# Performance work log

Measured on AMD Instinct MI355X. Metric: run time of the kernel, lower is better.

Reference implementation:

```python
import jax, jax.numpy as jnp
import numpy as np

B, T, F, H, E = 256, 512, 32, 512, 32
NUM_TICKERS, PREDICT_DAYS = 5000, 30


def setup_inputs() -> dict:
    key = jax.random.key(0)
    ks = jax.random.split(key, 16)
    s = 0.05  # small init scale for stability
    return {
        "ticker_id": jax.random.randint(ks[0], (B,), 0, NUM_TICKERS),
        "sequence": jax.random.normal(ks[1], (B, T, F), jnp.float32),
        "embed_table": jax.random.normal(ks[2], (NUM_TICKERS, E), jnp.float32) * s,
        "Wih0": jax.random.normal(ks[3], (3 * H, F), jnp.float32) * s,
        "Whh0": jax.random.normal(ks[4], (3 * H, H), jnp.float32) * s,
        "bih0": jax.random.normal(ks[5], (3 * H,), jnp.float32) * s,
        "bhh0": jax.random.normal(ks[6], (3 * H,), jnp.float32) * s,
        "Wih1": jax.random.normal(ks[7], (3 * H, H), jnp.float32) * s,
        "Whh1": jax.random.normal(ks[8], (3 * H, H), jnp.float32) * s,
        "bih1": jax.random.normal(ks[9], (3 * H,), jnp.float32) * s,
        "bhh1": jax.random.normal(ks[10], (3 * H,), jnp.float32) * s,
        "fc1_w": jax.random.normal(ks[11], (H, H + E), jnp.float32) * s,
        "fc1_b": jax.random.normal(ks[12], (H,), jnp.float32) * s,
        "fc2_w": jax.random.normal(ks[13], (PREDICT_DAYS, H), jnp.float32) * s,
        "fc2_b": jax.random.normal(ks[14], (PREDICT_DAYS,), jnp.float32) * s,
    }


def _gru_layer(x, Wih, Whh, bih, bhh):
    """Standard torch-convention GRU layer. x: (B,T,in) -> (B,T,H), h_last (B,H).
    Gate packing along 3H axis: [r, z, n]."""
    Hs = Whh.shape[1]
    # precompute input projections for all timesteps in one GEMM
    gx = jnp.einsum('btf,gf->tbg', x, Wih) + bih  # (T,B,3H)

    def step(h, gxt):
        gh = h @ Whh.T + bhh                         # (B,3H)
        r = jax.nn.sigmoid(gxt[:, :Hs] + gh[:, :Hs])
        z = jax.nn.sigmoid(gxt[:, Hs:2 * Hs] + gh[:, Hs:2 * Hs])
        n = jnp.tanh(gxt[:, 2 * Hs:] + r * gh[:, 2 * Hs:])
        h_new = (1.0 - z) * n + z * h
        return h_new, h_new

    h0 = jnp.zeros((x.shape[0], Hs), x.dtype)
    h_last, ys = jax.lax.scan(step, h0, gx)          # ys: (T,B,H)
    return jnp.moveaxis(ys, 0, 1), h_last


def reference(ticker_id, sequence, embed_table, Wih0, Whh0, bih0, bhh0,
              Wih1, Whh1, bih1, bhh1, fc1_w, fc1_b, fc2_w, fc2_b):
    out0, _ = _gru_layer(sequence, Wih0, Whh0, bih0, bhh0)
    _, h_last = _gru_layer(out0, Wih1, Whh1, bih1, bhh1)   # top-layer final hidden (B,H)
    embed = embed_table[ticker_id]                          # (B,E)
    h = jnp.concatenate([h_last, embed], axis=1)            # (B,H+E)
    h = jax.nn.relu(h @ fc1_w.T + fc1_b)                    # dropout is eval no-op
    return h @ fc2_w.T + fc2_b                              # (B, predict_days)
```

## Files before the change

### kernel.cpp

```cpp
#include <hip/hip_runtime.h>
#include <hip/hip_bf16.h>


namespace {
constexpr int kB  = 256;
constexpr int kT  = 512;
constexpr int kF  = 32;
constexpr int kH  = 512;
constexpr int kE  = 32;
constexpr int kPD = 30;

constexpr int GBLK = 256;
constexpr int NTHR = 256;
constexpr int RG   = 32;
constexpr int HB   = 16;

constexpr int IMG  = kB * kH * 2;
constexpr int RING = 8;

constexpr int PART_OFF = 0;
constexpr int PARTN    = 1536;
constexpr int LDSB     = 98304;
static_assert(LDSB <= 160 * 1024, "LDS overflow");

constexpr size_t WS_CNT   = 0;
constexpr size_t WS_TOTAL = 1024;
constexpr size_t WS_FB    = 1152;
constexpr size_t WS_FLG1  = 2048;
constexpr size_t WS_FLG0  = 4096;
constexpr size_t WS_H0B   = 65536;
constexpr size_t WS_H1B   = WS_H0B + (size_t)RING * IMG;
constexpr size_t WS_H1F   = WS_H1B + (size_t)RING * IMG;
constexpr size_t WS_INIT  = WS_H1F;

typedef __bf16 bf16_t;
typedef __bf16 bf16x8 __attribute__((ext_vector_type(8)));
typedef float  f32x4  __attribute__((ext_vector_type(4)));

#define MFMA __builtin_amdgcn_mfma_f32_16x16x32_bf16
#define LDSF4(p) (*(__attribute__((address_space(3))) f32x4*)(p))

#define WAITVM(N)                                              \
  do {                                                         \
    asm volatile("s_waitcnt vmcnt(" #N ")" ::: "memory");      \
    __builtin_amdgcn_sched_barrier(0);                         \
  } while (0)

__device__ __forceinline__ float sigmoid_f(float x) {
  return 1.f / (1.f + __expf(-x));
}
__device__ __forceinline__ float tanh_f(float x) {
  float a = fabsf(x);
  float e = __expf(-2.f * a);
  float t = (1.f - e) / (1.f + e);
  return copysignf(t, x);
}

__device__ __forceinline__ bf16x8 ld16a(const char* p) {
  bf16x8 v;
  asm volatile("global_load_dwordx4 %0, %1, off"
               : "=v"(v) : "v"(p) : "memory");
  return v;
}

__device__ __forceinline__ bf16x8 fragf(const float* p) {
  bf16x8 t;
#pragma unroll
  for (int j = 0; j < 8; ++j) t[j] = (bf16_t)p[j];
  return t;
}

__device__ __forceinline__ bf16x8 ld16_mall(const bf16_t* p) {
  const unsigned long long* q = (const unsigned long long*)p;
  unsigned long long lo =
      __hip_atomic_load(q, __ATOMIC_RELAXED, __HIP_MEMORY_SCOPE_AGENT);
  unsigned long long hi =
      __hip_atomic_load(q + 1, __ATOMIC_RELAXED, __HIP_MEMORY_SCOPE_AGENT);
  union { unsigned long long u[2]; bf16x8 v; } x;
  x.u[0] = lo; x.u[1] = hi;
  return x.v;
}

__device__ __forceinline__ void st2_mall(bf16_t* p, float v) {
  bf16_t b = (bf16_t)v;
  unsigned short bits = __builtin_bit_cast(unsigned short, b);
  __hip_atomic_store((unsigned short*)p, bits, __ATOMIC_RELAXED,
                     __HIP_MEMORY_SCOPE_AGENT);
}
template <bool XL>
__device__ __forceinline__ void st2x(bf16_t* p, float v) {
  if constexpr (XL) *p = (bf16_t)v;
  else st2_mall(p, v);
}

__device__ __forceinline__ void drain_stores() {
  asm volatile("s_waitcnt vmcnt(0)" ::: "memory");
}

__device__ __forceinline__ unsigned ld_flag_sc1(const unsigned* p) {
  unsigned v;
  asm volatile("global_load_dword %0, %1, off sc1\n\ts_waitcnt vmcnt(0)"
               : "=v"(v) : "v"(p) : "memory");
  return v;
}

template <bool XL>
__device__ __forceinline__ void poll_flags(const unsigned* base, int idx,
                                           unsigned tgt) {
  const unsigned* fp = base + idx;
  long guard = 0;
  if constexpr (XL) {
    for (;;) {
      unsigned v = ld_flag_sc1(fp);
      if (__all((int)(v >= tgt))) break;
      if (++guard > (1L << 22)) break;
    }
  } else {
    for (;;) {
      unsigned v = __hip_atomic_load(fp, __ATOMIC_RELAXED,
                                     __HIP_MEMORY_SCOPE_AGENT);
      if (__all((int)(v >= tgt))) break;
      __builtin_amdgcn_s_sleep(1);
      if (++guard > (1L << 20)) break;
    }
  }
}

template <bool XL>
__device__ __forceinline__ void flag_post(unsigned* p, unsigned tgt) {
  if constexpr (XL) {
    *(volatile unsigned*)p = tgt;
  } else {
    __hip_atomic_store(p, tgt, __ATOMIC_RELAXED, __HIP_MEMORY_SCOPE_AGENT);
  }
}
}


#define L0_ISSUE(buf, base)                                         \
  _Pragma("unroll") for (int j = 0; j < 4; ++j)                     \
      buf[j] = ld16a(hsrc + (base + j) * 1024)
#define L0_MFMA(buf, base)                                          \
  _Pragma("unroll") for (int j = 0; j < 4; ++j) {                   \
    aR  = MFMA(buf[j], f0[0][base + j], aR, 0, 0, 0);               \
    aZ  = MFMA(buf[j], f0[1][base + j], aZ, 0, 0, 0);               \
    aNH = MFMA(buf[j], f0[2][base + j], aNH, 0, 0, 0);              \
  }
#define L1_ISSUE(b0, b1, base)                                      \
  _Pragma("unroll") for (int j = 0; j < 4; ++j) {                   \
    b0[j] = ld16a(hsrc + (base + j) * 1024);                        \
    b1[j] = ld16a(hsrc + 16384 + (base + j) * 1024);                \
  }
#define L1_MFMA(acc0, acc1, acc2, w, b0, b1, base)                  \
  _Pragma("unroll") for (int j = 0; j < 4; ++j) {                   \
    acc0[0] = MFMA(b0[j], w[0][base + j], acc0[0], 0, 0, 0);        \
    acc0[1] = MFMA(b1[j], w[0][base + j], acc0[1], 0, 0, 0);        \
    acc1[0] = MFMA(b0[j], w[1][base + j], acc1[0], 0, 0, 0);        \
    acc1[1] = MFMA(b1[j], w[1][base + j], acc1[1], 0, 0, 0);        \
    acc2[0] = MFMA(b0[j], w[2][base + j], acc2[0], 0, 0, 0);        \
    acc2[1] = MFMA(b1[j], w[2][base + j], acc2[1], 0, 0, 0);        \
  }

template <bool XL>
__device__ __attribute__((noinline)) void role_l0(
    const float* __restrict__ seq, const float* __restrict__ Whh0,
    const float* __restrict__ Wih0, bf16_t* __restrict__ h0b,
    unsigned* __restrict__ flg0p, int g, int slot, int lane, int rbase,
    int rt, int c, float b0r, float b0z, float b0nx, float b0nh) {
  const int lm = lane & 15, lq = lane >> 4, koff = lq * 8;
  const int arow = rbase + rt * 16 + lm;

  bf16x8 f0[3][17];
#pragma unroll
  for (int gg = 0; gg < 3; ++gg) {
    const float* wh = Whh0 + (size_t)(gg * kH + c) * kH + koff;
#pragma unroll
    for (int kc = 0; kc < 16; ++kc) f0[gg][kc] = fragf(wh + kc * 32);
    f0[gg][16] = fragf(Wih0 + (size_t)(gg * kH + c) * kF + koff);
  }
  float h0m[4] = {0.f, 0.f, 0.f, 0.f};

  const int kcb = slot >> 1;
  const int lq2 = ((slot & 1) << 1) | (lm >> 3);
  const int stoff = ((g * 2 + rt) * 16 + kcb) * 1024 +
                    ((lq2 << 4) + lq * 4) * 16 + (lm & 7) * 2;
  const int tbase = (g * 2 + rt) * 16 * 1024;

  for (int s = 0; s <= kT; ++s) {
    const int pr = (s + RING - 1) & (RING - 1), pw = s & (RING - 1);
    if (s < kT) {
      const float* xp = seq + ((size_t)arow * kT + s) * kF + koff;
      float xs[8];
#pragma unroll
      for (int j = 0; j < 8; ++j) xs[j] = xp[j];
      if (s > 0) poll_flags<XL>(flg0p, lane, (unsigned)s);
      if constexpr (XL) {
        if ((s & (RING - 1)) == 0) asm volatile("buffer_inv" ::: "memory");
      }
      f32x4 aR{0,0,0,0}, aZ{0,0,0,0}, aNH{0,0,0,0}, aNX{0,0,0,0};
      const char* hsrc = (const char*)h0b + pr * IMG + tbase + lane * 16;
      if constexpr (XL) {
        bf16x8 cA[4], cB[4];
        L0_ISSUE(cA, 0);
        L0_ISSUE(cB, 4);
        WAITVM(4);
        L0_MFMA(cA, 0);
        L0_ISSUE(cA, 8);
        WAITVM(4);
        L0_MFMA(cB, 4);
        L0_ISSUE(cB, 12);
        WAITVM(4);
        L0_MFMA(cA, 8);
        WAITVM(0);
        L0_MFMA(cB, 12);
      } else {
#pragma unroll
        for (int kc = 0; kc < 16; ++kc) {
          bf16x8 a = ld16_mall((const bf16_t*)(hsrc + kc * 1024));
          aR  = MFMA(a, f0[0][kc], aR, 0, 0, 0);
          aZ  = MFMA(a, f0[1][kc], aZ, 0, 0, 0);
          aNH = MFMA(a, f0[2][kc], aNH, 0, 0, 0);
        }
      }
      {
        bf16x8 ax;
#pragma unroll
        for (int j = 0; j < 8; ++j) ax[j] = (bf16_t)xs[j];
        aR  = MFMA(ax, f0[0][16], aR, 0, 0, 0);
        aZ  = MFMA(ax, f0[1][16], aZ, 0, 0, 0);
        aNX = MFMA(ax, f0[2][16], aNX, 0, 0, 0);
      }
      char* hnb = (char*)h0b + pw * IMG;
#pragma unroll
      for (int i = 0; i < 4; ++i) {
        float r = sigmoid_f(aR[i] + b0r);
        float z = sigmoid_f(aZ[i] + b0z);
        float n = tanh_f((aNX[i] + b0nx) + r * (aNH[i] + b0nh));
        float hn = (1.f - z) * n + z * h0m[i];
        h0m[i] = hn;
        st2x<XL>((bf16_t*)(hnb + stoff + i * 16), hn);
      }
      drain_stores();
      if (lane == 0) flag_post<XL>(flg0p + rt * 32 + slot, (unsigned)(s + 1));
    }
    __syncthreads();
    if constexpr (!XL) __syncthreads();
  }
}

template <bool XL>
__device__ __attribute__((noinline)) void role_l1h(
    const float* __restrict__ Whh1, bf16_t* __restrict__ h1b,
    float* __restrict__ h1f, unsigned* __restrict__ flg1p, int slot,
    float* part, int g, int lane, int rbase, int c,
    float b1r, float b1z, float b1nx, float b1nh) {
  const int lm = lane & 15, lq = lane >> 4, koff = lq * 8;
  bf16x8 fh[3][16];
#pragma unroll
  for (int gg = 0; gg < 3; ++gg) {
    const float* wh = Whh1 + (size_t)(gg * kH + c) * kH + koff;
#pragma unroll
    for (int kc = 0; kc < 16; ++kc) fh[gg][kc] = fragf(wh + kc * 32);
  }
  float h1m[2][4] = {{0,0,0,0},{0,0,0,0}};

  const int kcb = slot >> 1;
  const int lq2 = ((slot & 1) << 1) | (lm >> 3);
  const int st0 = (g * 2 * 16 + kcb) * 1024 +
                  ((lq2 << 4) + lq * 4) * 16 + (lm & 7) * 2;
  const int tbase = g * 2 * 16 * 1024;

  for (int s = 0; s <= kT; ++s) {
    const int pr = (s + RING - 1) & (RING - 1), pw = s & (RING - 1);
    f32x4 cR[2], cZ[2], cNH[2];
#pragma unroll
    for (int rt = 0; rt < 2; ++rt) {
      cR[rt] = f32x4{0,0,0,0}; cZ[rt] = f32x4{0,0,0,0}; cNH[rt] = f32x4{0,0,0,0};
    }
    if (s >= 1) {
      poll_flags<XL>(flg1p, lane & 31, (unsigned)s);
      if constexpr (XL) {
        if ((s & (RING - 1)) == 0) asm volatile("buffer_inv" ::: "memory");
      }
      const char* hsrc = (const char*)h1b + pr * IMG + tbase + lane * 16;
      if constexpr (XL) {
        bf16x8 a0A[4], a1A[4], a0B[4], a1B[4];
        L1_ISSUE(a0A, a1A, 0);
        L1_ISSUE(a0B, a1B, 4);
        WAITVM(8);
        L1_MFMA(cR, cZ, cNH, fh, a0A, a1A, 0);
        L1_ISSUE(a0A, a1A, 8);
        WAITVM(8);
        L1_MFMA(cR, cZ, cNH, fh, a0B, a1B, 4);
        L1_ISSUE(a0B, a1B, 12);
        WAITVM(8);
        L1_MFMA(cR, cZ, cNH, fh, a0A, a1A, 8);
        WAITVM(0);
        L1_MFMA(cR, cZ, cNH, fh, a0B, a1B, 12);
      } else {
#pragma unroll
        for (int kc = 0; kc < 16; ++kc) {
          bf16x8 a0 = ld16_mall((const bf16_t*)(hsrc + kc * 1024));
          bf16x8 a1 = ld16_mall((const bf16_t*)(hsrc + 16384 + kc * 1024));
          cR[0]  = MFMA(a0, fh[0][kc], cR[0], 0,0,0);
          cR[1]  = MFMA(a1, fh[0][kc], cR[1], 0,0,0);
          cZ[0]  = MFMA(a0, fh[1][kc], cZ[0], 0,0,0);
          cZ[1]  = MFMA(a1, fh[1][kc], cZ[1], 0,0,0);
          cNH[0] = MFMA(a0, fh[2][kc], cNH[0],0,0,0);
          cNH[1] = MFMA(a1, fh[2][kc], cNH[1],0,0,0);
        }
      }
    }
    __syncthreads();
    if (s >= 1) {
      float* pb = part + (s & 1) * PARTN;
      char* hnb = (char*)h1b + pw * IMG;
#pragma unroll
      for (int rt = 0; rt < 2; ++rt) {
        f32x4 pR  = LDSF4(pb + ((rt * 3 + 0) * 64 + lane) * 4);
        f32x4 pZ  = LDSF4(pb + ((rt * 3 + 1) * 64 + lane) * 4);
        f32x4 pNX = LDSF4(pb + ((rt * 3 + 2) * 64 + lane) * 4);
#pragma unroll
        for (int i = 0; i < 4; ++i) {
          float r = sigmoid_f(cR[rt][i] + pR[i] + b1r);
          float z = sigmoid_f(cZ[rt][i] + pZ[i] + b1z);
          float n = tanh_f((pNX[i] + b1nx) + r * (cNH[rt][i] + b1nh));
          float hn = (1.f - z) * n + z * h1m[rt][i];
          h1m[rt][i] = hn;
          if (s < kT) st2x<XL>((bf16_t*)(hnb + st0 + rt * 16384 + i * 16), hn);
          else        h1f[(rbase + rt * 16 + lq * 4 + i) * kH + c] = hn;
        }
      }
    }
    if (s < kT) {
      drain_stores();
      if (lane == 0) flag_post<XL>(flg1p + slot, (unsigned)(s + 1));
    }
    if constexpr (!XL) {
      if (s < kT) poll_flags<XL>(flg1p, lane & 31, (unsigned)(s + 1));
      __syncthreads();
    }
  }
}

template <bool XL>
__device__ __attribute__((noinline)) void role_l1x(
    const float* __restrict__ Wih1, bf16_t* __restrict__ h0b,
    float* part, unsigned* __restrict__ flg0p, int g, int lane, int c) {
  const int lq = lane >> 4, koff = lq * 8;
  bf16x8 fx[3][16];
#pragma unroll
  for (int gg = 0; gg < 3; ++gg) {
    const float* wi = Wih1 + (size_t)(gg * kH + c) * kH + koff;
#pragma unroll
    for (int kc = 0; kc < 16; ++kc) fx[gg][kc] = fragf(wi + kc * 32);
  }
  const int tbase = g * 2 * 16 * 1024;

  for (int s = 0; s <= kT; ++s) {
    const int pr = (s + RING - 1) & (RING - 1);
    if (s >= 1) {
      poll_flags<XL>(flg0p, lane, (unsigned)s);
      if constexpr (XL) {
        if ((s & (RING - 1)) == 0) asm volatile("buffer_inv" ::: "memory");
      }
      f32x4 xR[2], xZ[2], xNX[2];
#pragma unroll
      for (int rt = 0; rt < 2; ++rt) {
        xR[rt] = f32x4{0,0,0,0}; xZ[rt] = f32x4{0,0,0,0}; xNX[rt] = f32x4{0,0,0,0};
      }
      const char* hsrc = (const char*)h0b + pr * IMG + tbase + lane * 16;
      if constexpr (XL) {
        bf16x8 a0A[4], a1A[4], a0B[4], a1B[4];
        L1_ISSUE(a0A, a1A, 0);
        L1_ISSUE(a0B, a1B, 4);
        WAITVM(8);
        L1_MFMA(xR, xZ, xNX, fx, a0A, a1A, 0);
        L1_ISSUE(a0A, a1A, 8);
        WAITVM(8);
        L1_MFMA(xR, xZ, xNX, fx, a0B, a1B, 4);
        L1_ISSUE(a0B, a1B, 12);
        WAITVM(8);
        L1_MFMA(xR, xZ, xNX, fx, a0A, a1A, 8);
        WAITVM(0);
        L1_MFMA(xR, xZ, xNX, fx, a0B, a1B, 12);
      } else {
#pragma unroll
        for (int kc = 0; kc < 16; ++kc) {
          bf16x8 a0 = ld16_mall((const bf16_t*)(hsrc + kc * 1024));
          bf16x8 a1 = ld16_mall((const bf16_t*)(hsrc + 16384 + kc * 1024));
          xR[0]  = MFMA(a0, fx[0][kc], xR[0], 0,0,0);
          xR[1]  = MFMA(a1, fx[0][kc], xR[1], 0,0,0);
          xZ[0]  = MFMA(a0, fx[1][kc], xZ[0], 0,0,0);
          xZ[1]  = MFMA(a1, fx[1][kc], xZ[1], 0,0,0);
          xNX[0] = MFMA(a0, fx[2][kc], xNX[0],0,0,0);
          xNX[1] = MFMA(a1, fx[2][kc], xNX[1],0,0,0);
        }
      }
      float* pb = part + (s & 1) * PARTN;
#pragma unroll
      for (int rt = 0; rt < 2; ++rt) {
        LDSF4(pb + ((rt * 3 + 0) * 64 + lane) * 4) = xR[rt];
        LDSF4(pb + ((rt * 3 + 1) * 64 + lane) * 4) = xZ[rt];
        LDSF4(pb + ((rt * 3 + 2) * 64 + lane) * 4) = xNX[rt];
      }
    }
    __syncthreads();
    if constexpr (!XL) __syncthreads();
  }
}

__launch_bounds__(NTHR, 1)
__global__ void gru_persistent(
    const float* __restrict__ seq,
    const float* __restrict__ Wih0, const float* __restrict__ Whh0,
    const float* __restrict__ bih0, const float* __restrict__ bhh0,
    const float* __restrict__ Wih1, const float* __restrict__ Whh1,
    const float* __restrict__ bih1, const float* __restrict__ bhh1,
    char* __restrict__ ws) {
  extern __shared__ char smem[];
  float* part = (float*)(smem + PART_OFF);
  __shared__ unsigned sh_enc;

  const int tid = threadIdx.x;

  if (tid == 0) {
    unsigned xcd;
    asm("s_getreg_b32 %0, hwreg(HW_REG_XCC_ID)" : "=s"(xcd));
    xcd &= 7;
    unsigned* cnt   = (unsigned*)(ws + WS_CNT) + xcd * 32;
    unsigned* total = (unsigned*)(ws + WS_TOTAL);
    unsigned* fb    = (unsigned*)(ws + WS_FB);
    unsigned slot = __hip_atomic_fetch_add(cnt, 1u, __ATOMIC_RELAXED,
                                           __HIP_MEMORY_SCOPE_AGENT);
    if (slot >= 32)
      __hip_atomic_store(fb, 1u, __ATOMIC_RELAXED, __HIP_MEMORY_SCOPE_AGENT);
    __hip_atomic_fetch_add(total, 1u, __ATOMIC_RELAXED,
                           __HIP_MEMORY_SCOPE_AGENT);
    long guard = 0;
    while (__hip_atomic_load(total, __ATOMIC_RELAXED,
                             __HIP_MEMORY_SCOPE_AGENT) < (unsigned)GBLK) {
      __builtin_amdgcn_s_sleep(1);
      if (++guard > (1L << 24)) break;
    }
    unsigned f = __hip_atomic_load(fb, __ATOMIC_RELAXED,
                                   __HIP_MEMORY_SCOPE_AGENT);
    sh_enc = (f << 31) | (xcd << 8) | (slot & 255);
  }
  __syncthreads();
  const unsigned enc = sh_enc;
  const bool fallback = (enc >> 31) != 0;
  const int g    = fallback ? (blockIdx.x & 7)  : (int)((enc >> 8) & 7);
  const int slot = fallback ? (blockIdx.x >> 3) : (int)(enc & 255);
  const int hs   = slot * HB;

  const int lm = tid & 15;
  const int c = hs + lm;
  const float b0r  = bih0[c] + bhh0[c];
  const float b0z  = bih0[kH + c] + bhh0[kH + c];
  const float b0nx = bih0[2 * kH + c];
  const float b0nh = bhh0[2 * kH + c];
  const float b1r  = bih1[c] + bhh1[c];
  const float b1z  = bih1[kH + c] + bhh1[kH + c];
  const float b1nx = bih1[2 * kH + c];
  const float b1nh = bhh1[2 * kH + c];

  bf16_t* h0b = (bf16_t*)(ws + WS_H0B);
  bf16_t* h1b = (bf16_t*)(ws + WS_H1B);
  float*  h1f = (float*)(ws + WS_H1F);
  unsigned* flg1p = (unsigned*)(ws + WS_FLG1) + g * 32;
  unsigned* flg0p = (unsigned*)(ws + WS_FLG0) + g * 64;
  const int wv   = tid >> 6;
  const int lane = tid & 63;
  const int rbase = g * RG;

  if (!fallback) {
    if (wv == 0)
      role_l0<true>(seq, Whh0, Wih0, h0b, flg0p, g, slot, lane, rbase, 0, c,
                    b0r, b0z, b0nx, b0nh);
    else if (wv == 2)
      role_l0<true>(seq, Whh0, Wih0, h0b, flg0p, g, slot, lane, rbase, 1, c,
                    b0r, b0z, b0nx, b0nh);
    else if (wv == 1)
      role_l1h<true>(Whh1, h1b, h1f, flg1p, slot, part, g, lane, rbase, c,
                     b1r, b1z, b1nx, b1nh);
    else
      role_l1x<true>(Wih1, h0b, part, flg0p, g, lane, c);
  } else {
    if (wv == 0)
      role_l0<false>(seq, Whh0, Wih0, h0b, flg0p, g, slot, lane, rbase, 0, c,
                     b0r, b0z, b0nx, b0nh);
    else if (wv == 2)
      role_l0<false>(seq, Whh0, Wih0, h0b, flg0p, g, slot, lane, rbase, 1, c,
                     b0r, b0z, b0nx, b0nh);
    else if (wv == 1)
      role_l1h<false>(Whh1, h1b, h1f, flg1p, slot, part, g, lane, rbase, c,
                      b1r, b1z, b1nx, b1nh);
    else
      role_l1x<false>(Wih1, h0b, part, flg0p, g, lane, c);
  }
}

__global__ void head_kernel(const float* __restrict__ h1,
                            const int* __restrict__ ticker,
                            const float* __restrict__ etab,
                            const float* __restrict__ fc1w,
                            const float* __restrict__ fc1b,
                            const float* __restrict__ fc2w,
                            const float* __restrict__ fc2b,
                            float* __restrict__ out) {
  __shared__ float xin[4][kH + kE];
  __shared__ float y1[4][kH];
  const int tid = threadIdx.x;
  const int b0 = blockIdx.x * 4;

  for (int idx = tid; idx < 4 * (kH + kE); idx += 256) {
    const int r = idx / (kH + kE), k = idx % (kH + kE);
    const int b = b0 + r;
    xin[r][k] = (k < kH) ? h1[b * kH + k] : etab[ticker[b] * kE + (k - kH)];
  }
  __syncthreads();

#pragma unroll
  for (int jj = 0; jj < 2; ++jj) {
    const int j = tid + jj * 256;
    const float* wr = fc1w + j * (kH + kE);
    float a0 = 0.f, a1 = 0.f, a2 = 0.f, a3 = 0.f;
    for (int k = 0; k < kH + kE; ++k) {
      const float w = wr[k];
      a0 += w * xin[0][k];
      a1 += w * xin[1][k];
      a2 += w * xin[2][k];
      a3 += w * xin[3][k];
    }
    const float bb = fc1b[j];
    y1[0][j] = fmaxf(a0 + bb, 0.f);
    y1[1][j] = fmaxf(a1 + bb, 0.f);
    y1[2][j] = fmaxf(a2 + bb, 0.f);
    y1[3][j] = fmaxf(a3 + bb, 0.f);
  }
  __syncthreads();

  if (tid < 4 * kPD) {
    const int r = tid / kPD, j = tid % kPD;
    const float* wr = fc2w + j * kH;
    float acc = fc2b[j];
    for (int k = 0; k < kH; ++k) acc += wr[k] * y1[r][k];
    out[(b0 + r) * kPD + j] = acc;
  }
}

extern "C" void kernel_launch(void* const* d_in, const int* in_sizes, int n_in,
                              void* d_out, int out_size, void* d_ws,
                              size_t ws_size, hipStream_t stream) {
  (void)in_sizes; (void)n_in; (void)out_size; (void)ws_size;

  const int*   ticker = (const int*)d_in[0];
  const float* seq    = (const float*)d_in[1];
  const float* etab   = (const float*)d_in[2];
  const float* Wih0   = (const float*)d_in[3];
  const float* Whh0   = (const float*)d_in[4];
  const float* bih0   = (const float*)d_in[5];
  const float* bhh0   = (const float*)d_in[6];
  const float* Wih1   = (const float*)d_in[7];
  const float* Whh1   = (const float*)d_in[8];
  const float* bih1   = (const float*)d_in[9];
  const float* bhh1   = (const float*)d_in[10];
  const float* fc1w   = (const float*)d_in[11];
  const float* fc1b   = (const float*)d_in[12];
  const float* fc2w   = (const float*)d_in[13];
  const float* fc2b   = (const float*)d_in[14];

  char* ws = (char*)d_ws;
  (void)hipMemsetAsync(ws, 0, WS_INIT, stream);

  gru_persistent<<<GBLK, NTHR, LDSB, stream>>>(
      seq, Wih0, Whh0, bih0, bhh0, Wih1, Whh1, bih1, bhh1, ws);

  head_kernel<<<kB / 4, 256, 0, stream>>>((const float*)(ws + WS_H1F), ticker,
                                          etab, fc1w, fc1b, fc2w, fc2b,
                                          (float*)d_out);
}
```

Baseline: 2.178 ms.

## Split each recurrent role across two waves with LDS partial-sum handoff

Doubles the block to 512 threads and splits every role (layer-0 recurrence, layer-1 hidden and input projections) across a lead wave and a partner wave. Each wave handles half of the K dimension, and partner partial sums reach the lead through double-buffered LDS slots guarded by LDS mailbox counters. The aim is to halve the serial per-step MFMA and load chain on the latency-bound recurrence and to halve weight-fragment register pressure. The cost is extra LDS traffic and intra-block spin-wait handshakes on every timestep.

Measured after the change: 2.626 ms. 1.21x slower.

```diff
diff --git a/kernel.cpp b/kernel.cpp
--- a/kernel.cpp
+++ b/kernel.cpp
@@ -11,16 +11,19 @@
 constexpr int kPD = 30;
 
 constexpr int GBLK = 256;
-constexpr int NTHR = 256;
+constexpr int NTHR = 512;
 constexpr int RG   = 32;
 constexpr int HB   = 16;
 
 constexpr int IMG  = kB * kH * 2;
 constexpr int RING = 8;
 
-constexpr int PART_OFF = 0;
-constexpr int PARTN    = 1536;
-constexpr int LDSB     = 98304;
+constexpr int PB0_OFF = 0;
+constexpr int PB2_OFF = 8192;
+constexpr int PB1_OFF = 16384;
+constexpr int PB3_OFF = 32768;
+constexpr int HS_OFF  = 61440;
+constexpr int LDSB    = 98304;
 static_assert(LDSB <= 160 * 1024, "LDS overflow");
 
 constexpr size_t WS_CNT   = 0;
@@ -39,6 +42,7 @@
 
 #define MFMA __builtin_amdgcn_mfma_f32_16x16x32_bf16
 #define LDSF4(p) (*(__attribute__((address_space(3))) f32x4*)(p))
+#define LDSVU(p) (*(volatile __attribute__((address_space(3))) unsigned*)(p))
 
 #define WAITVM(N)                                              \
   do {                                                         \
@@ -134,24 +138,32 @@
     __hip_atomic_store(p, tgt, __ATOMIC_RELAXED, __HIP_MEMORY_SCOPE_AGENT);
   }
 }
-}
-
-
-#define L0_ISSUE(buf, base)                                         \
+
+__device__ __forceinline__ void lds_poll(unsigned* p, unsigned tgt) {
+  long guard = 0;
+  while (LDSVU(p) < tgt) {
+    if (++guard > (1L << 22)) break;
+  }
+  asm volatile("" ::: "memory");
+}
+}
+
+
+#define HL0_ISSUE(buf, base)                                        \
   _Pragma("unroll") for (int j = 0; j < 4; ++j)                     \
       buf[j] = ld16a(hsrc + (base + j) * 1024)
-#define L0_MFMA(buf, base)                                          \
+#define HL0_MFMA(w, buf, base)                                      \
   _Pragma("unroll") for (int j = 0; j < 4; ++j) {                   \
-    aR  = MFMA(buf[j], f0[0][base + j], aR, 0, 0, 0);               \
-    aZ  = MFMA(buf[j], f0[1][base + j], aZ, 0, 0, 0);               \
-    aNH = MFMA(buf[j], f0[2][base + j], aNH, 0, 0, 0);              \
-  }
-#define L1_ISSUE(b0, b1, base)                                      \
+    aR  = MFMA(buf[j], w[0][base + j], aR, 0, 0, 0);                \
+    aZ  = MFMA(buf[j], w[1][base + j], aZ, 0, 0, 0);                \
+    aNH = MFMA(buf[j], w[2][base + j], aNH, 0, 0, 0);               \
+  }
+#define HL1_ISSUE(b0, b1, base)                                     \
   _Pragma("unroll") for (int j = 0; j < 4; ++j) {                   \
     b0[j] = ld16a(hsrc + (base + j) * 1024);                        \
     b1[j] = ld16a(hsrc + 16384 + (base + j) * 1024);                \
   }
-#define L1_MFMA(acc0, acc1, acc2, w, b0, b1, base)                  \
+#define HL1_MFMA(acc0, acc1, acc2, w, b0, b1, base)                 \
   _Pragma("unroll") for (int j = 0; j < 4; ++j) {                   \
     acc0[0] = MFMA(b0[j], w[0][base + j], acc0[0], 0, 0, 0);        \
     acc0[1] = MFMA(b1[j], w[0][base + j], acc0[1], 0, 0, 0);        \
@@ -162,58 +174,97 @@
   }
 
 template <bool XL>
-__device__ __attribute__((noinline)) void role_l0(
+__device__ __attribute__((noinline)) void role_l0_lead(
     const float* __restrict__ seq, const float* __restrict__ Whh0,
     const float* __restrict__ Wih0, bf16_t* __restrict__ h0b,
-    unsigned* __restrict__ flg0p, int g, int slot, int lane, int rbase,
-    int rt, int c, float b0r, float b0z, float b0nx, float b0nh) {
+    unsigned* __restrict__ flg0p, unsigned* mb, unsigned* pd, float* pbuf,
+    int g, int slot, int lane, int rbase, int rt, int c,
+    float b0r, float b0z, float b0nx, float b0nh) {
   const int lm = lane & 15, lq = lane >> 4, koff = lq * 8;
   const int arow = rbase + rt * 16 + lm;
-
-  bf16x8 f0[3][17];
-#pragma unroll
-  for (int gg = 0; gg < 3; ++gg) {
-    const float* wh = Whh0 + (size_t)(gg * kH + c) * kH + koff;
-#pragma unroll
-    for (int kc = 0; kc < 16; ++kc) f0[gg][kc] = fragf(wh + kc * 32);
-    f0[gg][16] = fragf(Wih0 + (size_t)(gg * kH + c) * kF + koff);
-  }
-  float h0m[4] = {0.f, 0.f, 0.f, 0.f};
-
   const int kcb = slot >> 1;
   const int lq2 = ((slot & 1) << 1) | (lm >> 3);
   const int stoff = ((g * 2 + rt) * 16 + kcb) * 1024 +
                     ((lq2 << 4) + lq * 4) * 16 + (lm & 7) * 2;
   const int tbase = (g * 2 + rt) * 16 * 1024;
-
-  for (int s = 0; s <= kT; ++s) {
-    const int pr = (s + RING - 1) & (RING - 1), pw = s & (RING - 1);
-    if (s < kT) {
-      const float* xp = seq + ((size_t)arow * kT + s) * kF + koff;
-      float xs[8];
-#pragma unroll
-      for (int j = 0; j < 8; ++j) xs[j] = xp[j];
-      if (s > 0) poll_flags<XL>(flg0p, lane, (unsigned)s);
-      if constexpr (XL) {
+  float h0m[4] = {0.f, 0.f, 0.f, 0.f};
+
+  if constexpr (XL) {
+    bf16x8 f0[3][9];
+#pragma unroll
+    for (int gg = 0; gg < 3; ++gg) {
+      const float* wh = Whh0 + (size_t)(gg * kH + c) * kH + koff;
+#pragma unroll
+      for (int kc = 0; kc < 8; ++kc) f0[gg][kc] = fragf(wh + kc * 32);
+      f0[gg][8] = fragf(Wih0 + (size_t)(gg * kH + c) * kF + koff);
+    }
+    for (int s = 0; s <= kT; ++s) {
+      const int pr = (s + RING - 1) & (RING - 1), pw = s & (RING - 1);
+      if (s < kT) {
+        const float* xp = seq + ((size_t)arow * kT + s) * kF + koff;
+        float xs[8];
+#pragma unroll
+        for (int j = 0; j < 8; ++j) xs[j] = xp[j];
+        if (s > 0) poll_flags<XL>(flg0p, lane, (unsigned)s);
         if ((s & (RING - 1)) == 0) asm volatile("buffer_inv" ::: "memory");
-      }
-      f32x4 aR{0,0,0,0}, aZ{0,0,0,0}, aNH{0,0,0,0}, aNX{0,0,0,0};
-      const char* hsrc = (const char*)h0b + pr * IMG + tbase + lane * 16;
-      if constexpr (XL) {
+        if (lane == 0) LDSVU(mb) = (unsigned)(s + 1);
+        f32x4 aR{0,0,0,0}, aZ{0,0,0,0}, aNH{0,0,0,0}, aNX{0,0,0,0};
+        const char* hsrc = (const char*)h0b + pr * IMG + tbase + lane * 16;
         bf16x8 cA[4], cB[4];
-        L0_ISSUE(cA, 0);
-        L0_ISSUE(cB, 4);
+        HL0_ISSUE(cA, 0);
+        HL0_ISSUE(cB, 4);
         WAITVM(4);
-        L0_MFMA(cA, 0);
-        L0_ISSUE(cA, 8);
-        WAITVM(4);
-        L0_MFMA(cB, 4);
-        L0_ISSUE(cB, 12);
-        WAITVM(4);
-        L0_MFMA(cA, 8);
+        HL0_MFMA(f0, cA, 0);
         WAITVM(0);
-        L0_MFMA(cB, 12);
-      } else {
+        HL0_MFMA(f0, cB, 4);
+        {
+          bf16x8 ax;
+#pragma unroll
+          for (int j = 0; j < 8; ++j) ax[j] = (bf16_t)xs[j];
+          aR  = MFMA(ax, f0[0][8], aR, 0, 0, 0);
+          aZ  = MFMA(ax, f0[1][8], aZ, 0, 0, 0);
+          aNX = MFMA(ax, f0[2][8], aNX, 0, 0, 0);
+        }
+        lds_poll(pd, (unsigned)(s + 1));
+        float* pp = pbuf + (s & 1) * 768;
+        aR  += LDSF4(pp + (0 * 64 + lane) * 4);
+        aZ  += LDSF4(pp + (1 * 64 + lane) * 4);
+        aNH += LDSF4(pp + (2 * 64 + lane) * 4);
+        char* hnb = (char*)h0b + pw * IMG;
+#pragma unroll
+        for (int i = 0; i < 4; ++i) {
+          float r = sigmoid_f(aR[i] + b0r);
+          float z = sigmoid_f(aZ[i] + b0z);
+          float n = tanh_f((aNX[i] + b0nx) + r * (aNH[i] + b0nh));
+          float hn = (1.f - z) * n + z * h0m[i];
+          h0m[i] = hn;
+          st2x<XL>((bf16_t*)(hnb + stoff + i * 16), hn);
+        }
+        drain_stores();
+        if (lane == 0)
+          flag_post<XL>(flg0p + rt * 32 + slot, (unsigned)(s + 1));
+      }
+      __syncthreads();
+    }
+  } else {
+    bf16x8 f0[3][17];
+#pragma unroll
+    for (int gg = 0; gg < 3; ++gg) {
+      const float* wh = Whh0 + (size_t)(gg * kH + c) * kH + koff;
+#pragma unroll
+      for (int kc = 0; kc < 16; ++kc) f0[gg][kc] = fragf(wh + kc * 32);
+      f0[gg][16] = fragf(Wih0 + (size_t)(gg * kH + c) * kF + koff);
+    }
+    for (int s = 0; s <= kT; ++s) {
+      const int pr = (s + RING - 1) & (RING - 1), pw = s & (RING - 1);
+      if (s < kT) {
+        const float* xp = seq + ((size_t)arow * kT + s) * kF + koff;
+        float xs[8];
+#pragma unroll
+        for (int j = 0; j < 8; ++j) xs[j] = xp[j];
+        if (s > 0) poll_flags<XL>(flg0p, lane, (unsigned)s);
+        f32x4 aR{0,0,0,0}, aZ{0,0,0,0}, aNH{0,0,0,0}, aNX{0,0,0,0};
+        const char* hsrc = (const char*)h0b + pr * IMG + tbase + lane * 16;
 #pragma unroll
         for (int kc = 0; kc < 16; ++kc) {
           bf16x8 a = ld16_mall((const bf16_t*)(hsrc + kc * 1024));
@@ -221,83 +272,174 @@
           aZ  = MFMA(a, f0[1][kc], aZ, 0, 0, 0);
           aNH = MFMA(a, f0[2][kc], aNH, 0, 0, 0);
         }
-      }
-      {
         bf16x8 ax;
 #pragma unroll
         for (int j = 0; j < 8; ++j) ax[j] = (bf16_t)xs[j];
         aR  = MFMA(ax, f0[0][16], aR, 0, 0, 0);
         aZ  = MFMA(ax, f0[1][16], aZ, 0, 0, 0);
         aNX = MFMA(ax, f0[2][16], aNX, 0, 0, 0);
-      }
-      char* hnb = (char*)h0b + pw * IMG;
-#pragma unroll
-      for (int i = 0; i < 4; ++i) {
-        float r = sigmoid_f(aR[i] + b0r);
-        float z = sigmoid_f(aZ[i] + b0z);
-        float n = tanh_f((aNX[i] + b0nx) + r * (aNH[i] + b0nh));
-        float hn = (1.f - z) * n + z * h0m[i];
-        h0m[i] = hn;
-        st2x<XL>((bf16_t*)(hnb + stoff + i * 16), hn);
-      }
-      drain_stores();
-      if (lane == 0) flag_post<XL>(flg0p + rt * 32 + slot, (unsigned)(s + 1));
-    }
-    __syncthreads();
-    if constexpr (!XL) __syncthreads();
+        char* hnb = (char*)h0b + pw * IMG;
+#pragma unroll
+        for (int i = 0; i < 4; ++i) {
+          float r = sigmoid_f(aR[i] + b0r);
+          float z = sigmoid_f(aZ[i] + b0z);
+          float n = tanh_f((aNX[i] + b0nx) + r * (aNH[i] + b0nh));
+          float hn = (1.f - z) * n + z * h0m[i];
+          h0m[i] = hn;
+          st2x<XL>((bf16_t*)(hnb + stoff + i * 16), hn);
+        }
+        drain_stores();
+        if (lane == 0)
+          flag_post<XL>(flg0p + rt * 32 + slot, (unsigned)(s + 1));
+      }
+      __syncthreads();
+      __syncthreads();
+    }
   }
 }
 
 template <bool XL>
-__device__ __attribute__((noinline)) void role_l1h(
+__device__ __attribute__((noinline)) void role_l0_part(
+    const float* __restrict__ Whh0, bf16_t* __restrict__ h0b,
+    unsigned* mb, unsigned* pd, float* pbuf,
+    int g, int lane, int rt, int c) {
+  if constexpr (XL) {
+    const int lq = lane >> 4, koff = lq * 8;
+    bf16x8 f4[3][8];
+#pragma unroll
+    for (int gg = 0; gg < 3; ++gg) {
+      const float* wh = Whh0 + (size_t)(gg * kH + c) * kH + koff;
+#pragma unroll
+      for (int kc = 0; kc < 8; ++kc) f4[gg][kc] = fragf(wh + (8 + kc) * 32);
+    }
+    const int tbase = (g * 2 + rt) * 16 * 1024;
+    for (int s = 0; s <= kT; ++s) {
+      const int pr = (s + RING - 1) & (RING - 1);
+      if (s < kT) {
+        lds_poll(mb, (unsigned)(s + 1));
+        if ((s & (RING - 1)) == 0) asm volatile("buffer_inv" ::: "memory");
+        f32x4 aR{0,0,0,0}, aZ{0,0,0,0}, aNH{0,0,0,0};
+        const char* hsrc =
+            (const char*)h0b + pr * IMG + tbase + 8192 + lane * 16;
+        bf16x8 cA[4], cB[4];
+        HL0_ISSUE(cA, 0);
+        HL0_ISSUE(cB, 4);
+        WAITVM(4);
+        HL0_MFMA(f4, cA, 0);
+        WAITVM(0);
+        HL0_MFMA(f4, cB, 4);
+        float* pp = pbuf + (s & 1) * 768;
+        LDSF4(pp + (0 * 64 + lane) * 4) = aR;
+        LDSF4(pp + (1 * 64 + lane) * 4) = aZ;
+        LDSF4(pp + (2 * 64 + lane) * 4) = aNH;
+        asm volatile("s_waitcnt lgkmcnt(0)" ::: "memory");
+        if (lane == 0) LDSVU(pd) = (unsigned)(s + 1);
+      }
+      __syncthreads();
+    }
+  } else {
+    for (int s = 0; s <= kT; ++s) { __syncthreads(); __syncthreads(); }
+  }
+}
+
+template <bool XL>
+__device__ __attribute__((noinline)) void role_l1h_lead(
     const float* __restrict__ Whh1, bf16_t* __restrict__ h1b,
     float* __restrict__ h1f, unsigned* __restrict__ flg1p, int slot,
-    float* part, int g, int lane, int rbase, int c,
+    float* p1b, float* p3b, unsigned* mb, int g, int lane, int rbase, int c,
     float b1r, float b1z, float b1nx, float b1nh) {
   const int lm = lane & 15, lq = lane >> 4, koff = lq * 8;
-  bf16x8 fh[3][16];
-#pragma unroll
-  for (int gg = 0; gg < 3; ++gg) {
-    const float* wh = Whh1 + (size_t)(gg * kH + c) * kH + koff;
-#pragma unroll
-    for (int kc = 0; kc < 16; ++kc) fh[gg][kc] = fragf(wh + kc * 32);
-  }
-  float h1m[2][4] = {{0,0,0,0},{0,0,0,0}};
-
   const int kcb = slot >> 1;
   const int lq2 = ((slot & 1) << 1) | (lm >> 3);
   const int st0 = (g * 2 * 16 + kcb) * 1024 +
                   ((lq2 << 4) + lq * 4) * 16 + (lm & 7) * 2;
   const int tbase = g * 2 * 16 * 1024;
-
-  for (int s = 0; s <= kT; ++s) {
-    const int pr = (s + RING - 1) & (RING - 1), pw = s & (RING - 1);
-    f32x4 cR[2], cZ[2], cNH[2];
-#pragma unroll
-    for (int rt = 0; rt < 2; ++rt) {
-      cR[rt] = f32x4{0,0,0,0}; cZ[rt] = f32x4{0,0,0,0}; cNH[rt] = f32x4{0,0,0,0};
-    }
-    if (s >= 1) {
-      poll_flags<XL>(flg1p, lane & 31, (unsigned)s);
-      if constexpr (XL) {
+  float h1m[2][4] = {{0,0,0,0},{0,0,0,0}};
+
+  if constexpr (XL) {
+    bf16x8 fh[3][8];
+#pragma unroll
+    for (int gg = 0; gg < 3; ++gg) {
+      const float* wh = Whh1 + (size_t)(gg * kH + c) * kH + koff;
+#pragma unroll
+      for (int kc = 0; kc < 8; ++kc) fh[gg][kc] = fragf(wh + kc * 32);
+    }
+    for (int s = 0; s <= kT; ++s) {
+      const int pr = (s + RING - 1) & (RING - 1), pw = s & (RING - 1);
+      f32x4 cR[2], cZ[2], cNH[2];
+#pragma unroll
+      for (int rt = 0; rt < 2; ++rt) {
+        cR[rt] = f32x4{0,0,0,0}; cZ[rt] = f32x4{0,0,0,0};
+        cNH[rt] = f32x4{0,0,0,0};
+      }
+      if (s >= 1) {
+        poll_flags<XL>(flg1p, lane & 31, (unsigned)s);
         if ((s & (RING - 1)) == 0) asm volatile("buffer_inv" ::: "memory");
-      }
-      const char* hsrc = (const char*)h1b + pr * IMG + tbase + lane * 16;
-      if constexpr (XL) {
+        if (lane == 0) LDSVU(mb) = (unsigned)(s + 1);
+        const char* hsrc = (const char*)h1b + pr * IMG + tbase + lane * 16;
         bf16x8 a0A[4], a1A[4], a0B[4], a1B[4];
-        L1_ISSUE(a0A, a1A, 0);
-        L1_ISSUE(a0B, a1B, 4);
+        HL1_ISSUE(a0A, a1A, 0);
+        HL1_ISSUE(a0B, a1B, 4);
         WAITVM(8);
-        L1_MFMA(cR, cZ, cNH, fh, a0A, a1A, 0);
-        L1_ISSUE(a0A, a1A, 8);
-        WAITVM(8);
-        L1_MFMA(cR, cZ, cNH, fh, a0B, a1B, 4);
-        L1_ISSUE(a0B, a1B, 12);
-        WAITVM(8);
-        L1_MFMA(cR, cZ, cNH, fh, a0A, a1A, 8);
+        HL1_MFMA(cR, cZ, cNH, fh, a0A, a1A, 0);
         WAITVM(0);
-        L1_MFMA(cR, cZ, cNH, fh, a0B, a1B, 12);
-      } else {
+        HL1_MFMA(cR, cZ, cNH, fh, a0B, a1B, 4);
+      }
+      __syncthreads();
+      if (s >= 1) {
+        float* p5 = p1b + (s & 1) * 1536;
+        float* pa = p3b + (s & 1) * 3072;
+        float* pb = pa + 1536;
+        char* hnb = (char*)h1b + pw * IMG;
+#pragma unroll
+        for (int rt = 0; rt < 2; ++rt) {
+          f32x4 cr = cR[rt]  + LDSF4(p5 + ((rt * 3 + 0) * 64 + lane) * 4);
+          f32x4 cz = cZ[rt]  + LDSF4(p5 + ((rt * 3 + 1) * 64 + lane) * 4);
+          f32x4 cn = cNH[rt] + LDSF4(p5 + ((rt * 3 + 2) * 64 + lane) * 4);
+          f32x4 pR  = LDSF4(pa + ((rt * 3 + 0) * 64 + lane) * 4) +
+                      LDSF4(pb + ((rt * 3 + 0) * 64 + lane) * 4);
+          f32x4 pZ  = LDSF4(pa + ((rt * 3 + 1) * 64 + lane) * 4) +
+                      LDSF4(pb + ((rt * 3 + 1) * 64 + lane) * 4);
+          f32x4 pNX = LDSF4(pa + ((rt * 3 + 2) * 64 + lane) * 4) +
+                      LDSF4(pb + ((rt * 3 + 2) * 64 + lane) * 4);
+#pragma unroll
+          for (int i = 0; i < 4; ++i) {
+            float r = sigmoid_f(cr[i] + pR[i] + b1r);
+            float z = sigmoid_f(cz[i] + pZ[i] + b1z);
+            float n = tanh_f((pNX[i] + b1nx) + r * (cn[i] + b1nh));
+            float hn = (1.f - z) * n + z * h1m[rt][i];
+            h1m[rt][i] = hn;
+            if (s < kT)
+              st2x<XL>((bf16_t*)(hnb + st0 + rt * 16384 + i * 16), hn);
+            else
+              h1f[(rbase + rt * 16 + lq * 4 + i) * kH + c] = hn;
+          }
+        }
+      }
+      if (s < kT) {
+        drain_stores();
+        if (lane == 0) flag_post<XL>(flg1p + slot, (unsigned)(s + 1));
+      }
+    }
+  } else {
+    bf16x8 fh[3][16];
+#pragma unroll
+    for (int gg = 0; gg < 3; ++gg) {
+      const float* wh = Whh1 + (size_t)(gg * kH + c) * kH + koff;
+#pragma unroll
+      for (int kc = 0; kc < 16; ++kc) fh[gg][kc] = fragf(wh + kc * 32);
+    }
+    for (int s = 0; s <= kT; ++s) {
+      const int pr = (s + RING - 1) & (RING - 1), pw = s & (RING - 1);
+      f32x4 cR[2], cZ[2], cNH[2];
+#pragma unroll
+      for (int rt = 0; rt < 2; ++rt) {
+        cR[rt] = f32x4{0,0,0,0}; cZ[rt] = f32x4{0,0,0,0};
+        cNH[rt] = f32x4{0,0,0,0};
+      }
+      if (s >= 1) {
+        poll_flags<XL>(flg1p, lane & 31, (unsigned)s);
+        const char* hsrc = (const char*)h1b + pr * IMG + tbase + lane * 16;
 #pragma unroll
         for (int kc = 0; kc < 16; ++kc) {
           bf16x8 a0 = ld16_mall((const bf16_t*)(hsrc + kc * 1024));
@@ -310,103 +452,185 @@
           cNH[1] = MFMA(a1, fh[2][kc], cNH[1],0,0,0);
         }
       }
-    }
-    __syncthreads();
-    if (s >= 1) {
-      float* pb = part + (s & 1) * PARTN;
-      char* hnb = (char*)h1b + pw * IMG;
-#pragma unroll
-      for (int rt = 0; rt < 2; ++rt) {
-        f32x4 pR  = LDSF4(pb + ((rt * 3 + 0) * 64 + lane) * 4);
-        f32x4 pZ  = LDSF4(pb + ((rt * 3 + 1) * 64 + lane) * 4);
-        f32x4 pNX = LDSF4(pb + ((rt * 3 + 2) * 64 + lane) * 4);
-#pragma unroll
-        for (int i = 0; i < 4; ++i) {
-          float r = sigmoid_f(cR[rt][i] + pR[i] + b1r);
-          float z = sigmoid_f(cZ[rt][i] + pZ[i] + b1z);
-          float n = tanh_f((pNX[i] + b1nx) + r * (cNH[rt][i] + b1nh));
-          float hn = (1.f - z) * n + z * h1m[rt][i];
-          h1m[rt][i] = hn;
-          if (s < kT) st2x<XL>((bf16_t*)(hnb + st0 + rt * 16384 + i * 16), hn);
-          else        h1f[(rbase + rt * 16 + lq * 4 + i) * kH + c] = hn;
-        }
-      }
-    }
-    if (s < kT) {
-      drain_stores();
-      if (lane == 0) flag_post<XL>(flg1p + slot, (unsigned)(s + 1));
-    }
-    if constexpr (!XL) {
-      if (s < kT) poll_flags<XL>(flg1p, lane & 31, (unsigned)(s + 1));
       __syncthreads();
+      if (s >= 1) {
+        float* pa = p3b + (s & 1) * 3072;
+        char* hnb = (char*)h1b + pw * IMG;
+#pragma unroll
+        for (int rt = 0; rt < 2; ++rt) {
+          f32x4 pR  = LDSF4(pa + ((rt * 3 + 0) * 64 + lane) * 4);
+          f32x4 pZ  = LDSF4(pa + ((rt * 3 + 1) * 64 + lane) * 4);
+          f32x4 pNX = LDSF4(pa + ((rt * 3 + 2) * 64 + lane) * 4);
+#pragma unroll
+          for (int i = 0; i < 4; ++i) {
+            float r = sigmoid_f(cR[rt][i] + pR[i] + b1r);
+            float z = sigmoid_f(cZ[rt][i] + pZ[i] + b1z);
+            float n = tanh_f((pNX[i] + b1nx) + r * (cNH[rt][i] + b1nh));
+            float hn = (1.f - z) * n + z * h1m[rt][i];
+            h1m[rt][i] = hn;
+            if (s < kT)
+              st2x<XL>((bf16_t*)(hnb + st0 + rt * 16384 + i * 16), hn);
+            else
+              h1f[(rbase + rt * 16 + lq * 4 + i) * kH + c] = hn;
+          }
+        }
+      }
+      if (s < kT) {
+        drain_stores();
+        if (lane == 0) flag_post<XL>(flg1p + slot, (unsigned)(s + 1));
+        poll_flags<XL>(flg1p, lane & 31, (unsigned)(s + 1));
+      }
+      __syncthreads();
     }
   }
 }
 
 template <bool XL>
-__device__ __attribute__((noinline)) void role_l1x(
+__device__ __attribute__((noinline)) void role_l1h_part(
+    const float* __restrict__ Whh1, bf16_t* __restrict__ h1b,
+    float* p1b, unsigned* mb, int g, int lane, int c) {
+  if constexpr (XL) {
+    const int lq = lane >> 4, koff = lq * 8;
+    bf16x8 fh[3][8];
+#pragma unroll
+    for (int gg = 0; gg < 3; ++gg) {
+      const float* wh = Whh1 + (size_t)(gg * kH + c) * kH + koff;
+#pragma unroll
+      for (int kc = 0; kc < 8; ++kc) fh[gg][kc] = fragf(wh + (8 + kc) * 32);
+    }
+    const int tbase = g * 2 * 16 * 1024;
+    for (int s = 0; s <= kT; ++s) {
+      const int pr = (s + RING - 1) & (RING - 1);
+      if (s >= 1) {
+        lds_poll(mb, (unsigned)(s + 1));
+        if ((s & (RING - 1)) == 0) asm volatile("buffer_inv" ::: "memory");
+        f32x4 cR[2], cZ[2], cNH[2];
+#pragma unroll
+        for (int rt = 0; rt < 2; ++rt) {
+          cR[rt] = f32x4{0,0,0,0}; cZ[rt] = f32x4{0,0,0,0};
+          cNH[rt] = f32x4{0,0,0,0};
+        }
+        const char* hsrc =
+            (const char*)h1b + pr * IMG + tbase + 8192 + lane * 16;
+        bf16x8 a0A[4], a1A[4], a0B[4], a1B[4];
+        HL1_ISSUE(a0A, a1A, 0);
+        HL1_ISSUE(a0B, a1B, 4);
+        WAITVM(8);
+        HL1_MFMA(cR, cZ, cNH, fh, a0A, a1A, 0);
+        WAITVM(0);
+        HL1_MFMA(cR, cZ, cNH, fh, a0B, a1B, 4);
+        float* pp = p1b + (s & 1) * 1536;
+#pragma unroll
+        for (int rt = 0; rt < 2; ++rt) {
+          LDSF4(pp + ((rt * 3 + 0) * 64 + lane) * 4) = cR[rt];
+          LDSF4(pp + ((rt * 3 + 1) * 64 + lane) * 4) = cZ[rt];
+          LDSF4(pp + ((rt * 3 + 2) * 64 + lane) * 4) = cNH[rt];
+        }
+      }
+      __syncthreads();
+    }
+  } else {
+    for (int s = 0; s <= kT; ++s) { __syncthreads(); __syncthreads(); }
+  }
+}
+
+template <bool XL, bool LEAD>
+__device__ __attribute__((noinline)) void role_l1x_w(
     const float* __restrict__ Wih1, bf16_t* __restrict__ h0b,
-    float* part, unsigned* __restrict__ flg0p, int g, int lane, int c) {
+    float* p3b, unsigned* __restrict__ flg0p, unsigned* mb,
+    int g, int lane, int c) {
   const int lq = lane >> 4, koff = lq * 8;
-  bf16x8 fx[3][16];
-#pragma unroll
-  for (int gg = 0; gg < 3; ++gg) {
-    const float* wi = Wih1 + (size_t)(gg * kH + c) * kH + koff;
-#pragma unroll
-    for (int kc = 0; kc < 16; ++kc) fx[gg][kc] = fragf(wi + kc * 32);
-  }
   const int tbase = g * 2 * 16 * 1024;
-
-  for (int s = 0; s <= kT; ++s) {
-    const int pr = (s + RING - 1) & (RING - 1);
-    if (s >= 1) {
-      poll_flags<XL>(flg0p, lane, (unsigned)s);
-      if constexpr (XL) {
-        if ((s & (RING - 1)) == 0) asm volatile("buffer_inv" ::: "memory");
-      }
-      f32x4 xR[2], xZ[2], xNX[2];
-#pragma unroll
-      for (int rt = 0; rt < 2; ++rt) {
-        xR[rt] = f32x4{0,0,0,0}; xZ[rt] = f32x4{0,0,0,0}; xNX[rt] = f32x4{0,0,0,0};
-      }
-      const char* hsrc = (const char*)h0b + pr * IMG + tbase + lane * 16;
-      if constexpr (XL) {
+  if constexpr (XL) {
+    bf16x8 fx[3][8];
+#pragma unroll
+    for (int gg = 0; gg < 3; ++gg) {
+      const float* wi = Wih1 + (size_t)(gg * kH + c) * kH + koff;
+#pragma unroll
+      for (int kc = 0; kc < 8; ++kc)
+        fx[gg][kc] = fragf(wi + (LEAD ? kc : 8 + kc) * 32);
+    }
+    for (int s = 0; s <= kT; ++s) {
+      const int pr = (s + RING - 1) & (RING - 1);
+      if (s >= 1) {
+        if constexpr (LEAD) {
+          poll_flags<XL>(flg0p, lane, (unsigned)s);
+          if ((s & (RING - 1)) == 0) asm volatile("buffer_inv" ::: "memory");
+          if (lane == 0) LDSVU(mb) = (unsigned)(s + 1);
+        } else {
+          lds_poll(mb, (unsigned)(s + 1));
+          if ((s & (RING - 1)) == 0) asm volatile("buffer_inv" ::: "memory");
+        }
+        f32x4 xR[2], xZ[2], xNX[2];
+#pragma unroll
+        for (int rt = 0; rt < 2; ++rt) {
+          xR[rt] = f32x4{0,0,0,0}; xZ[rt] = f32x4{0,0,0,0};
+          xNX[rt] = f32x4{0,0,0,0};
+        }
+        const char* hsrc = (const char*)h0b + pr * IMG + tbase +
+                           (LEAD ? 0 : 8192) + lane * 16;
         bf16x8 a0A[4], a1A[4], a0B[4], a1B[4];
-        L1_ISSUE(a0A, a1A, 0);
-        L1_ISSUE(a0B, a1B, 4);
+        HL1_ISSUE(a0A, a1A, 0);
+        HL1_ISSUE(a0B, a1B, 4);
         WAITVM(8);
-        L1_MFMA(xR, xZ, xNX, fx, a0A, a1A, 0);
-        L1_ISSUE(a0A, a1A, 8);
-        WAITVM(8);
-        L1_MFMA(xR, xZ, xNX, fx, a0B, a1B, 4);
-        L1_ISSUE(a0B, a1B, 12);
-        WAITVM(8);
-        L1_MFMA(xR, xZ, xNX, fx, a0A, a1A, 8);
+        HL1_MFMA(xR, xZ, xNX, fx, a0A, a1A, 0);
         WAITVM(0);
-        L1_MFMA(xR, xZ, xNX, fx, a0B, a1B, 12);
-      } else {
-#pragma unroll
-        for (int kc = 0; kc < 16; ++kc) {
-          bf16x8 a0 = ld16_mall((const bf16_t*)(hsrc + kc * 1024));
-          bf16x8 a1 = ld16_mall((const bf16_t*)(hsrc + 16384 + kc * 1024));
-          xR[0]  = MFMA(a0, fx[0][kc], xR[0], 0,0,0);
-          xR[1]  = MFMA(a1, fx[0][kc], xR[1], 0,0,0);
-          xZ[0]  = MFMA(a0, fx[1][kc], xZ[0], 0,0,0);
-          xZ[1]  = MFMA(a1, fx[1][kc], xZ[1], 0,0,0);
-          xNX[0] = MFMA(a0, fx[2][kc], xNX[0],0,0,0);
-          xNX[1] = MFMA(a1, fx[2][kc], xNX[1],0,0,0);
-        }
-      }
-      float* pb = part + (s & 1) * PARTN;
-#pragma unroll
-      for (int rt = 0; rt < 2; ++rt) {
-        LDSF4(pb + ((rt * 3 + 0) * 64 + lane) * 4) = xR[rt];
-        LDSF4(pb + ((rt * 3 + 1) * 64 + lane) * 4) = xZ[rt];
-        LDSF4(pb + ((rt * 3 + 2) * 64 + lane) * 4) = xNX[rt];
-      }
-    }
-    __syncthreads();
-    if constexpr (!XL) __syncthreads();
+        HL1_MFMA(xR, xZ, xNX, fx, a0B, a1B, 4);
+        float* pp = p3b + (s & 1) * 3072 + (LEAD ? 0 : 1536);
+#pragma unroll
+        for (int rt = 0; rt < 2; ++rt) {
+          LDSF4(pp + ((rt * 3 + 0) * 64 + lane) * 4) = xR[rt];
+          LDSF4(pp + ((rt * 3 + 1) * 64 + lane) * 4) = xZ[rt];
+          LDSF4(pp + ((rt * 3 + 2) * 64 + lane) * 4) = xNX[rt];
+        }
+      }
+      __syncthreads();
+    }
+  } else {
+    if constexpr (LEAD) {
+      bf16x8 fx[3][16];
+#pragma unroll
+      for (int gg = 0; gg < 3; ++gg) {
+        const float* wi = Wih1 + (size_t)(gg * kH + c) * kH + koff;
+#pragma unroll
+        for (int kc = 0; kc < 16; ++kc) fx[gg][kc] = fragf(wi + kc * 32);
+      }
+      for (int s = 0; s <= kT; ++s) {
+        const int pr = (s + RING - 1) & (RING - 1);
+        if (s >= 1) {
+          poll_flags<XL>(flg0p, lane, (unsigned)s);
+          f32x4 xR[2], xZ[2], xNX[2];
+#pragma unroll
+          for (int rt = 0; rt < 2; ++rt) {
+            xR[rt] = f32x4{0,0,0,0}; xZ[rt] = f32x4{0,0,0,0};
+            xNX[rt] = f32x4{0,0,0,0};
+          }
+          const char* hsrc = (const char*)h0b + pr * IMG + tbase + lane * 16;
+#pragma unroll
+          for (int kc = 0; kc < 16; ++kc) {
+            bf16x8 a0 = ld16_mall((const bf16_t*)(hsrc + kc * 1024));
+            bf16x8 a1 = ld16_mall((const bf16_t*)(hsrc + 16384 + kc * 1024));
+            xR[0]  = MFMA(a0, fx[0][kc], xR[0], 0,0,0);
+            xR[1]  = MFMA(a1, fx[0][kc], xR[1], 0,0,0);
+            xZ[0]  = MFMA(a0, fx[1][kc], xZ[0], 0,0,0);
+            xZ[1]  = MFMA(a1, fx[1][kc], xZ[1], 0,0,0);
+            xNX[0] = MFMA(a0, fx[2][kc], xNX[0],0,0,0);
+            xNX[1] = MFMA(a1, fx[2][kc], xNX[1],0,0,0);
+          }
+          float* pp = p3b + (s & 1) * 3072;
+#pragma unroll
+          for (int rt = 0; rt < 2; ++rt) {
+            LDSF4(pp + ((rt * 3 + 0) * 64 + lane) * 4) = xR[rt];
+            LDSF4(pp + ((rt * 3 + 1) * 64 + lane) * 4) = xZ[rt];
+            LDSF4(pp + ((rt * 3 + 2) * 64 + lane) * 4) = xNX[rt];
+          }
+        }
+        __syncthreads();
+        __syncthreads();
+      }
+    } else {
+      for (int s = 0; s <= kT; ++s) { __syncthreads(); __syncthreads(); }
+    }
   }
 }
 
@@ -419,12 +643,23 @@
     const float* __restrict__ bih1, const float* __restrict__ bhh1,
     char* __restrict__ ws) {
   extern __shared__ char smem[];
-  float* part = (float*)(smem + PART_OFF);
+  float* pb0 = (float*)(smem + PB0_OFF);
+  float* pb2 = (float*)(smem + PB2_OFF);
+  float* pb1 = (float*)(smem + PB1_OFF);
+  float* pb3 = (float*)(smem + PB3_OFF);
+  unsigned* mb0 = (unsigned*)(smem + HS_OFF + 0);
+  unsigned* pd0 = (unsigned*)(smem + HS_OFF + 128);
+  unsigned* mb2 = (unsigned*)(smem + HS_OFF + 256);
+  unsigned* pd2 = (unsigned*)(smem + HS_OFF + 384);
+  unsigned* mb1 = (unsigned*)(smem + HS_OFF + 512);
+  unsigned* mb3 = (unsigned*)(smem + HS_OFF + 640);
   __shared__ unsigned sh_enc;
 
   const int tid = threadIdx.x;
 
   if (tid == 0) {
+    LDSVU(mb0) = 0u; LDSVU(pd0) = 0u; LDSVU(mb2) = 0u;
+    LDSVU(pd2) = 0u; LDSVU(mb1) = 0u; LDSVU(mb3) = 0u;
     unsigned xcd;
     asm("s_getreg_b32 %0, hwreg(HW_REG_XCC_ID)" : "=s"(xcd));
     xcd &= 7;
@@ -474,31 +709,32 @@
   const int lane = tid & 63;
   const int rbase = g * RG;
 
-  if (!fallback) {
-    if (wv == 0)
-      role_l0<true>(seq, Whh0, Wih0, h0b, flg0p, g, slot, lane, rbase, 0, c,
-                    b0r, b0z, b0nx, b0nh);
-    else if (wv == 2)
-      role_l0<true>(seq, Whh0, Wih0, h0b, flg0p, g, slot, lane, rbase, 1, c,
-                    b0r, b0z, b0nx, b0nh);
-    else if (wv == 1)
-      role_l1h<true>(Whh1, h1b, h1f, flg1p, slot, part, g, lane, rbase, c,
-                     b1r, b1z, b1nx, b1nh);
-    else
-      role_l1x<true>(Wih1, h0b, part, flg0p, g, lane, c);
-  } else {
-    if (wv == 0)
-      role_l0<false>(seq, Whh0, Wih0, h0b, flg0p, g, slot, lane, rbase, 0, c,
-                     b0r, b0z, b0nx, b0nh);
-    else if (wv == 2)
-      role_l0<false>(seq, Whh0, Wih0, h0b, flg0p, g, slot, lane, rbase, 1, c,
-                     b0r, b0z, b0nx, b0nh);
-    else if (wv == 1)
-      role_l1h<false>(Whh1, h1b, h1f, flg1p, slot, part, g, lane, rbase, c,
-                      b1r, b1z, b1nx, b1nh);
-    else
-      role_l1x<false>(Wih1, h0b, part, flg0p, g, lane, c);
-  }
+#define DISPATCH(XLV)                                                       \
+  do {                                                                      \
+    if (wv == 0)                                                            \
+      role_l0_lead<XLV>(seq, Whh0, Wih0, h0b, flg0p, mb0, pd0, pb0, g,      \
+                        slot, lane, rbase, 0, c, b0r, b0z, b0nx, b0nh);     \
+    else if (wv == 4)                                                       \
+      role_l0_part<XLV>(Whh0, h0b, mb0, pd0, pb0, g, lane, 0, c);           \
+    else if (wv == 2)                                                       \
+      role_l0_lead<XLV>(seq, Whh0, Wih0, h0b, flg0p, mb2, pd2, pb2, g,      \
+                        slot, lane, rbase, 1, c, b0r, b0z, b0nx, b0nh);     \
+    else if (wv == 6)                                                       \
+      role_l0_part<XLV>(Whh0, h0b, mb2, pd2, pb2, g, lane, 1, c);           \
+    else if (wv == 1)                                                       \
+      role_l1h_lead<XLV>(Whh1, h1b, h1f, flg1p, slot, pb1, pb3, mb1, g,     \
+                         lane, rbase, c, b1r, b1z, b1nx, b1nh);             \
+    else if (wv == 5)                                                       \
+      role_l1h_part<XLV>(Whh1, h1b, pb1, mb1, g, lane, c);                  \
+    else if (wv == 3)                                                       \
+      role_l1x_w<XLV, true>(Wih1, h0b, pb3, flg0p, mb3, g, lane, c);        \
+    else                                                                    \
+      role_l1x_w<XLV, false>(Wih1, h0b, pb3, flg0p, mb3, g, lane, c);       \
+  } while (0)
+
+  if (!fallback) DISPATCH(true);
+  else           DISPATCH(false);
+#undef DISPATCH
 }
 
 __global__ void head_kernel(const float* __restrict__ h1,
```
